# Kernel tuning notes

Measured on AMD Instinct MI355X. Metric: run time of the kernel, lower is better.

## Reference

```python
import jax, jax.numpy as jnp
import numpy as np

# Dimensions derived from LaneATTHead defaults (see shape_source)
B, CIN, CF, FH, FW = 8, 256, 64, 22, 40
A, S = 2784, 72          # n_anchors, n_offsets
NC = 2                   # num_category
D = CF * FH              # per-anchor feature dim = 1408
P = NC + 2 + 2 * S       # proposal dim = 148


def setup_inputs() -> dict:
    key = jax.random.key(0)
    ks = jax.random.split(key, 12)
    sc = 0.02
    return {
        "x": jax.random.normal(ks[0], (B, CIN, FH, FW), jnp.float32),
        "conv_w": jax.random.normal(ks[1], (CF, CIN), jnp.float32) * sc,
        "conv_b": jax.random.normal(ks[2], (CF,), jnp.float32) * sc,
        "attn_w": jax.random.normal(ks[3], (D, A - 1), jnp.float32) * sc,
        "attn_b": jax.random.normal(ks[4], (A - 1,), jnp.float32) * sc,
        "cls_w": jax.random.normal(ks[5], (2 * D, NC), jnp.float32) * sc,
        "cls_b": jax.random.normal(ks[6], (NC,), jnp.float32) * sc,
        "reg_w": jax.random.normal(ks[7], (2 * D, 2 * S), jnp.float32) * sc,
        "reg_b": jax.random.normal(ks[8], (2 * S,), jnp.float32) * sc,
        "anchors": jax.random.uniform(ks[9], (A, P), jnp.float32),
        "cut_xs": jax.random.randint(ks[10], (A, FH), 0, FW, jnp.int32),
        "invalid_mask": jax.random.randint(ks[11], (A, FH), 0, 2, jnp.int32).astype(jnp.bool_),
    }


def reference(x, conv_w, conv_b, attn_w, attn_b, cls_w, cls_b, reg_w, reg_b,
              anchors, cut_xs, invalid_mask):
    # 1x1 conv: [B,CIN,FH,FW] -> [B,CF,FH,FW]
    feats = jnp.einsum('bchw,oc->bohw', x, conv_w) + conv_b[None, :, None, None]

    # cut_anchor_features: gather per-anchor column per row, zero invalid
    rows = jnp.arange(FH)
    g = feats[:, :, rows[None, :], cut_xs]             # [B, CF, A, FH]
    g = jnp.transpose(g, (0, 2, 1, 3))                  # [B, A, CF, FH]
    g = jnp.where(invalid_mask[None, :, None, :], jnp.float32(0), g)
    baf = g.reshape(B, A, D)                            # [B, A, D]

    # attention over other anchors (softmax over A-1 slots)
    scores = baf @ attn_w + attn_b                      # [B, A, A-1]
    attention = jax.nn.softmax(scores, axis=-1)

    # scatter into [A,A] with zero diagonal (row-major off-diag fill, as in eye()+nonzero())
    i = jnp.arange(A)[:, None]
    k = jnp.arange(A - 1)[None, :]
    cols = k + (k >= i).astype(jnp.int32)               # [A, A-1]
    attn_mat = jnp.zeros((B, A, A), baf.dtype).at[:, i, cols].set(attention)

    # weighted pooling (equiv. of the transposed bmm chain)
    att_feat = jnp.einsum('bij,bjd->bid', attn_mat, baf)  # [B, A, D]

    f2 = jnp.concatenate([att_feat, baf], axis=-1)      # [B, A, 2D]
    cls = f2 @ cls_w + cls_b                            # [B, A, NC]
    reg = f2 @ reg_w + reg_b                            # [B, A, 2S]
    reg = jnp.concatenate([reg[..., :S], jax.nn.sigmoid(reg[..., S:])], axis=-1)

    base = jnp.broadcast_to(anchors, (B, A, P))
    # reg_proposals: [:, :, :NC]=cls ; [:, :, NC:NC+2]=anchor ; [:, :, NC+2:]+=reg
    props = jnp.concatenate([cls, base[..., NC:NC + 2], base[..., NC + 2:] + reg], axis=-1)
    return props, attn_mat
```

## Files before the change

kernel.cpp:

```cpp
#include <hip/hip_runtime.h>
#include <stdint.h>

typedef __attribute__((ext_vector_type(8))) __bf16 bf16x8;
typedef __attribute__((ext_vector_type(4))) float f32x4;
typedef __attribute__((ext_vector_type(2))) long long2v;
typedef unsigned short u16;
typedef unsigned char u8;

#define DEV static __device__ __forceinline__

constexpr int NB = 8;
constexpr int AA = 2784;
constexpr int AM1 = 2783;
constexpr int DD = 1408;
constexpr int MT = NB * AA;
constexpr int KP = 2816;

DEV u16 f2bf(float f) {
  uint32_t u = __builtin_bit_cast(uint32_t, f);
  u += 0x7FFFu + ((u >> 16) & 1u);
  return (u16)(u >> 16);
}
DEV float bf2f(unsigned v) { return __builtin_bit_cast(float, v << 16); }
DEV u8 f2f8(float f) {
  return (u8)(__builtin_amdgcn_cvt_pk_fp8_f32(f, f, 0, false) & 0xff);
}
DEV float4 cv4(unsigned w) {
  float4 r;
  r.x = __builtin_amdgcn_cvt_f32_fp8((int)w, 0);
  r.y = __builtin_amdgcn_cvt_f32_fp8((int)w, 1);
  r.z = __builtin_amdgcn_cvt_f32_fp8((int)w, 2);
  r.w = __builtin_amdgcn_cvt_f32_fp8((int)w, 3);
  return r;
}
DEV unsigned pk4(float a, float b, float c, float d) {
  int r = __builtin_amdgcn_cvt_pk_fp8_f32(a, b, 0, false);
  r = __builtin_amdgcn_cvt_pk_fp8_f32(c, d, r, true);
  return (unsigned)r;
}

DEV void load16_lds(const void* g, void* l) {
  auto gp = (const __attribute__((address_space(1))) uint32_t*)(uintptr_t)g;
  auto lp = (__attribute__((address_space(3))) uint32_t*)(uint32_t)(uintptr_t)l;
  __builtin_amdgcn_global_load_lds(gp, lp, 16, 0, 0);
}

#define VMW(n) asm volatile("s_waitcnt vmcnt(" #n ")" ::: "memory")
#define VMW0 asm volatile("s_waitcnt vmcnt(0)" ::: "memory")
#define LGK(n) asm volatile("s_waitcnt lgkmcnt(" #n ")" ::: "memory")
#define BARR asm volatile("s_barrier" ::: "memory")
#define SCHB __builtin_amdgcn_sched_barrier(0)

DEV void mf16c(f32x4 (&acc)[4][2], const long (&a)[4][2], const long (&b)[2][2]) {
  __builtin_amdgcn_s_setprio(1);
#pragma unroll
  for (int mt = 0; mt < 4; ++mt)
#pragma unroll
    for (int nt = 0; nt < 2; ++nt)
#pragma unroll
      for (int ks = 0; ks < 2; ++ks)
        acc[mt][nt] = __builtin_amdgcn_mfma_f32_16x16x32_fp8_fp8(
            a[mt][ks], b[nt][ks], acc[mt][nt], 0, 0, 0);
  __builtin_amdgcn_s_setprio(0);
}

template <int MODE>
__global__ __launch_bounds__(512, 4) void gemm_k(const u8* __restrict__ A,
                                                 const u8* __restrict__ Bt,
                                                 u8* __restrict__ out8,
                                                 u16* __restrict__ outh,
                                                 const float* __restrict__ bias1) {
  constexpr int K   = (MODE == 1) ? 1408 : KP;
  constexpr int NT  = K / 128;
  constexpr int LDA = (MODE == 1) ? 1408 : KP;
  constexpr int LDB = (MODE == 1) ? 1408 : KP;
  constexpr int MR  = (MODE == 1) ? MT : AA;
  constexpr int NRB = (MODE == 1) ? KP : 1408;
  __shared__ __align__(16) u8 As8[2][16384];
  __shared__ __align__(16) u8 Bs8[2][16384];
  const int tid = threadIdx.x;
  const int lane = tid & 63;
  const int w = tid >> 6;
  const int wr = w >> 2, wc = w & 3;
  const int l16 = lane & 15, lq = lane >> 4;
  const int l7 = l16 & 7;

  const int gx = gridDim.x, gy = gridDim.y;
  const int nwg = gx * gy;
  const int i = blockIdx.x + blockIdx.y * gx;
  const int xcd = i & 7, pos = i >> 3;
  const int q = nwg >> 3, r = nwg & 7;
  const int lid = (xcd < r ? xcd * (q + 1) : r * (q + 1) + (xcd - r) * q) + pos;
  const int m0 = (lid / gy) * 128, n0 = (lid % gy) * 128;

  const u8* Ab = A;
  const u8* Bb = Bt;
  u16* outp = outh;
  if constexpr (MODE == 2) {
    const int bz = blockIdx.z;
    Ab += (size_t)bz * AA * KP;
    Bb += (size_t)bz * DD * KP;
    outp += (size_t)bz * AA * DD;
  }

  auto stA = [&](int buf, int kt) {
#pragma unroll
    for (int inst = 0; inst < 2; ++inst) {
      int c = tid + inst * 512;
      int row = c >> 3, sl = c & 7;
      int sr = m0 + row;
      sr = sr < MR - 1 ? sr : MR - 1;
      load16_lds(Ab + (size_t)sr * LDA + kt * 128 + ((sl ^ (row & 7)) << 4),
                 &As8[buf][c << 4]);
    }
  };
  auto stB = [&](int buf, int kt) {
#pragma unroll
    for (int inst = 0; inst < 2; ++inst) {
      int c = tid + inst * 512;
      int row = c >> 3, sl = c & 7;
      int sr = n0 + row;
      sr = sr < NRB - 1 ? sr : NRB - 1;
      load16_lds(Bb + (size_t)sr * LDB + kt * 128 + ((sl ^ (row & 7)) << 4),
                 &Bs8[buf][c << 4]);
    }
  };
  auto rdA = [&](int buf, int kh, long (&a)[4][2]) {
    const int u = (kh * 4 + lq) ^ l7;
#pragma unroll
    for (int mt = 0; mt < 4; ++mt) {
      int rloc = wr * 64 + mt * 16 + l16;
      long2v v = *(const long2v*)&As8[buf][rloc * 128 + u * 16];
      a[mt][0] = v[0]; a[mt][1] = v[1];
    }
  };
  auto rdB = [&](int buf, int kh, long (&b)[2][2]) {
    const int u = (kh * 4 + lq) ^ l7;
#pragma unroll
    for (int nt = 0; nt < 2; ++nt) {
      int R = wc * 32 + nt * 16 + l16;
      long2v v = *(const long2v*)&Bs8[buf][R * 128 + u * 16];
      b[nt][0] = v[0]; b[nt][1] = v[1];
    }
  };

  f32x4 acc[4][2];
#pragma unroll
  for (int i2 = 0; i2 < 4; ++i2)
#pragma unroll
    for (int j = 0; j < 2; ++j) acc[i2][j] = 0.f;

  long a[4][2], bA[2][2], bB[2][2];

  stA(0, 0); stB(0, 0);
  stA(1, 1); stB(1, 1);
  VMW(4);
  BARR;

  for (int t = 0; t < NT; ++t) {
    const int cur = t & 1, nxt = cur ^ 1;
    if (t + 1 < NT) { stA(nxt, t + 1); stB(nxt, t + 1); }
    rdB(cur, 0, bA); rdA(cur, 0, a); rdB(cur, 1, bB);
    LGK(2); SCHB;
    mf16c(acc, a, bA);
    rdA(cur, 1, a);
    LGK(0); SCHB;
    mf16c(acc, a, bB);
    if (t + 1 < NT) { VMW0; BARR; }
  }

  if constexpr (MODE == 1) {
#pragma unroll
    for (int mi = 0; mi < 4; ++mi)
#pragma unroll
      for (int r2 = 0; r2 < 4; ++r2) {
        int m = m0 + wr * 64 + mi * 16 + lq * 4 + r2;
        int ii = m % AA;
#pragma unroll
        for (int ni = 0; ni < 2; ++ni) {
          int n = n0 + wc * 32 + ni * 16 + l16;
          if (n >= AM1) continue;
          int col = n + (n >= ii);
          out8[(size_t)m * KP + col] = f2f8(acc[mi][ni][r2] + bias1[n]);
        }
      }
  } else {
#pragma unroll
    for (int mi = 0; mi < 4; ++mi)
#pragma unroll
      for (int r2 = 0; r2 < 4; ++r2) {
        int m = m0 + wr * 64 + mi * 16 + lq * 4 + r2;
        if (m >= AA) continue;
        size_t base = (size_t)m * DD;
#pragma unroll
        for (int ni = 0; ni < 2; ++ni) {
          int n = n0 + wc * 32 + ni * 16 + l16;
          outp[base + n] = f2bf(acc[mi][ni][r2] * 0.00390625f);
        }
      }
  }
}

__global__ __launch_bounds__(256) void conv_k(const float* __restrict__ x,
                                              const float* __restrict__ w,
                                              const float* __restrict__ bias,
                                              float* __restrict__ feats) {
  __shared__ float xs[256 * 40];
  int bb = blockIdx.x / 22, h = blockIdx.x % 22;
  const float* xp = x + (size_t)bb * 256 * 880 + h * 40;
  for (int l = threadIdx.x; l < 256 * 40; l += 256)
    xs[l] = xp[(l / 40) * 880 + (l % 40)];
  __syncthreads();
  for (int l = threadIdx.x; l < 64 * 40; l += 256) {
    int o = l / 40, ww = l % 40;
    float acc = bias[o];
    const float* wr = w + o * 256;
#pragma unroll 8
    for (int c = 0; c < 256; ++c) acc += xs[c * 40 + ww] * wr[c];
    feats[((size_t)(bb * 64 + o) * 22 + h) * 40 + ww] = acc;
  }
}

__global__ __launch_bounds__(256) void gt_k(const float* __restrict__ feats,
                                            const int* __restrict__ cut,
                                            const u8* __restrict__ inv,
                                            u16* __restrict__ baf,
                                            u8* __restrict__ baf8,
                                            u8* __restrict__ bft8) {
  unsigned probe = 0;
#pragma unroll
  for (int t = 0; t < 10; ++t)
    probe |= (unsigned)inv[4 * t + 1] | (unsigned)inv[4 * t + 2] | (unsigned)inv[4 * t + 3];
  const bool is_u8 = (probe != 0);
  __shared__ u8 t8[64][65];
  int a0 = blockIdx.x * 64, d0 = blockIdx.y * 64, b = blockIdx.z;
  int tx = threadIdx.x & 63, ty = threadIdx.x >> 6;
  int d = d0 + tx, o = d / 22, h = d - o * 22;
  for (int r = ty; r < 64; r += 4) {
    int a = a0 + r;
    u8 f8 = 0;
    if (a < AA) {
      int msk = is_u8 ? (int)inv[a * 22 + h] : ((const int*)inv)[a * 22 + h];
      float v = 0.f;
      if (!msk) v = feats[((size_t)(b * 64 + o) * 22 + h) * 40 + cut[a * 22 + h]];
      baf[((size_t)b * AA + a) * DD + d] = f2bf(v);
      f8 = f2f8(v);
      baf8[((size_t)b * AA + a) * DD + d] = f8;
    }
    t8[r][tx] = f8;
  }
  __syncthreads();
  for (int r = ty; r < 64; r += 4) {
    int a = a0 + tx;
    if (a < AA) bft8[((size_t)b * DD + d0 + r) * KP + a] = t8[tx][r];
  }
}

__global__ __launch_bounds__(256) void tr_attw_k(const float* __restrict__ w,
                                                 u8* __restrict__ wt8) {
  __shared__ u8 t8[64][65];
  int n0 = blockIdx.x * 64, k0 = blockIdx.y * 64;
  int tx = threadIdx.x & 63, ty = threadIdx.x >> 6;
  for (int r = ty; r < 64; r += 4) {
    int n = n0 + tx;
    t8[r][tx] = (n < AM1) ? f2f8(w[(size_t)(k0 + r) * AM1 + n]) : (u8)0;
  }
  __syncthreads();
  for (int r = ty; r < 64; r += 4)
    wt8[(size_t)(n0 + r) * 1408 + k0 + tx] = t8[tx][r];
}

__global__ __launch_bounds__(256) void wt_k(const float* __restrict__ cw,
                                            const float* __restrict__ rw,
                                            u16* __restrict__ wt) {
  int n = blockIdx.x;
  for (int k = threadIdx.x; k < 2816; k += 256) {
    float v = 0.f;
    if (n < 2) v = cw[(size_t)k * 2 + n];
    else if (n < 146) v = rw[(size_t)k * 144 + (n - 2)];
    wt[(size_t)n * 2816 + k] = f2bf(v);
  }
}

__global__ __launch_bounds__(256) void softf_k(u8* __restrict__ attP) {
  const int row = blockIdx.x;
  const int i = row % AA;
  u8* p = attP + (size_t)row * KP;
  const int t = threadIdx.x;
  const bool act = (t < 176);
  uint4 qw = act ? ((const uint4*)p)[t] : make_uint4(0, 0, 0, 0);
  float v[16];
  { float4 f = cv4(qw.x); v[0] = f.x; v[1] = f.y; v[2] = f.z; v[3] = f.w; }
  { float4 f = cv4(qw.y); v[4] = f.x; v[5] = f.y; v[6] = f.z; v[7] = f.w; }
  { float4 f = cv4(qw.z); v[8] = f.x; v[9] = f.y; v[10] = f.z; v[11] = f.w; }
  { float4 f = cv4(qw.w); v[12] = f.x; v[13] = f.y; v[14] = f.z; v[15] = f.w; }
  const int base = t * 16;
  float mx = -3e38f;
#pragma unroll
  for (int e = 0; e < 16; ++e) {
    int j = base + e;
    if (act && j < AA && j != i) mx = fmaxf(mx, v[e]);
  }
#pragma unroll
  for (int o = 1; o < 64; o <<= 1) mx = fmaxf(mx, __shfl_xor(mx, o));
  __shared__ float rm[4], rs[4];
  if (!(t & 63)) rm[t >> 6] = mx;
  __syncthreads();
  mx = fmaxf(fmaxf(rm[0], rm[1]), fmaxf(rm[2], rm[3]));
  float s = 0.f, ev[16];
#pragma unroll
  for (int e = 0; e < 16; ++e) {
    int j = base + e;
    float tv = (act && j < AA && j != i) ? __expf(v[e] - mx) : 0.f;
    ev[e] = tv; s += tv;
  }
#pragma unroll
  for (int o = 1; o < 64; o <<= 1) s += __shfl_xor(s, o);
  if (!(t & 63)) rs[t >> 6] = s;
  __syncthreads();
  s = (rs[0] + rs[1]) + (rs[2] + rs[3]);
  const float inv = 256.f / s;
#pragma unroll
  for (int e = 0; e < 16; ++e) ev[e] *= inv;
  if (act) {
    uint4 ow;
    ow.x = pk4(ev[0], ev[1], ev[2], ev[3]);
    ow.y = pk4(ev[4], ev[5], ev[6], ev[7]);
    ow.z = pk4(ev[8], ev[9], ev[10], ev[11]);
    ow.w = pk4(ev[12], ev[13], ev[14], ev[15]);
    ((uint4*)p)[t] = ow;
  }
}

__global__ __launch_bounds__(256) void exp_k(const u8* __restrict__ src,
                                             float* __restrict__ dst) {
  int row = blockIdx.x;
  int t = threadIdx.x;
  if (t >= 174) return;
  uint4 qw = ((const uint4*)(src + (size_t)row * KP))[t];
  const float is = 0.00390625f;
  float4 f0 = cv4(qw.x), f1 = cv4(qw.y), f2 = cv4(qw.z), f3 = cv4(qw.w);
  float4* dp = (float4*)(dst + (size_t)row * AA + t * 16);
  dp[0] = make_float4(f0.x * is, f0.y * is, f0.z * is, f0.w * is);
  dp[1] = make_float4(f1.x * is, f1.y * is, f1.z * is, f1.w * is);
  dp[2] = make_float4(f2.x * is, f2.y * is, f2.z * is, f2.w * is);
  dp[3] = make_float4(f3.x * is, f3.y * is, f3.z * is, f3.w * is);
}

__global__ __launch_bounds__(256) void head_k(const u16* __restrict__ A1,
                                              const u16* __restrict__ A2,
                                              const u16* __restrict__ Bt,
                                              float* __restrict__ outf,
                                              const float* __restrict__ b1,
                                              const float* __restrict__ b2,
                                              const float* __restrict__ anch) {
  constexpr int K = 2816, NT = K / 32, BN = 160, HN = 80, NF = 5;
  __shared__ __align__(16) u16 As[2][128 * 32];
  __shared__ __align__(16) u16 Bs[2][BN * 32 + 512];
  const int tid = threadIdx.x;
  const int lane = tid & 63;
  const int wm = tid >> 7, wn = (tid >> 6) & 1;
  const int m0 = blockIdx.x * 128;
  const int l16 = lane & 15, lq = lane >> 4;

  auto stage = [&](int buf, int t) {
    const int k0 = t * 32;
    const u16* Asrc = (k0 < 1408) ? A1 : A2;
    const int kk = (k0 < 1408) ? k0 : k0 - 1408;
#pragma unroll
    for (int inst = 0; inst < 2; ++inst) {
      int c = tid + inst * 256;
      load16_lds(Asrc + (size_t)(m0 + (c >> 2)) * 1408 + kk + (c & 3) * 8, &As[buf][c * 8]);
    }
#pragma unroll
    for (int inst = 0; inst < 3; ++inst) {
      int c = tid + inst * 256;
      int ce = c < BN * 4 ? c : BN * 4 - 1;
      load16_lds(Bt + (size_t)(ce >> 2) * K + k0 + (ce & 3) * 8, &Bs[buf][ce * 8]);
    }
  };

  f32x4 acc[4][NF];
#pragma unroll
  for (int i = 0; i < 4; ++i)
#pragma unroll
    for (int j = 0; j < NF; ++j) acc[i][j] = 0.f;

  stage(0, 0);
  stage(1, 1);
  for (int t = 0; t < NT; ++t) {
    if (t + 1 < NT) VMW(5); else VMW0;
    BARR;
    const int cur = t & 1;
    bf16x8 av[4], bv[NF];
#pragma unroll
    for (int mt = 0; mt < 4; ++mt)
      av[mt] = *(const bf16x8*)&As[cur][(wm * 64 + mt * 16 + l16) * 32 + lq * 8];
#pragma unroll
    for (int nt = 0; nt < NF; ++nt)
      bv[nt] = *(const bf16x8*)&Bs[cur][(wn * HN + nt * 16 + l16) * 32 + lq * 8];
#pragma unroll
    for (int mt = 0; mt < 4; ++mt)
#pragma unroll
      for (int nt = 0; nt < NF; ++nt)
        acc[mt][nt] = __builtin_amdgcn_mfma_f32_16x16x32_bf16(av[mt], bv[nt], acc[mt][nt], 0, 0, 0);
    BARR;
    if (t + 2 < NT) stage(cur, t + 2);
  }

#pragma unroll
  for (int nt = 0; nt < NF; ++nt) {
    int n = wn * HN + nt * 16 + l16;
    if (n >= 146) continue;
#pragma unroll
    for (int mt = 0; mt < 4; ++mt)
#pragma unroll
      for (int r = 0; r < 4; ++r) {
        int m = m0 + wm * 64 + mt * 16 + lq * 4 + r;
        int ii = m % AA;
        float v = acc[mt][nt][r];
        if (n < 2) {
          outf[(size_t)m * 148 + n] = v + b1[n];
          if (n == 0) {
            outf[(size_t)m * 148 + 2] = anch[ii * 148 + 2];
            outf[(size_t)m * 148 + 3] = anch[ii * 148 + 3];
          }
        } else {
          int rr = n - 2;
          v += b2[rr];
          if (rr >= 72) v = 1.f / (1.f + __expf(-v));
          outf[(size_t)m * 148 + 4 + rr] = anch[ii * 148 + 4 + rr] + v;
        }
      }
  }
}

extern "C" void kernel_launch(void* const* d_in, const int* in_sizes, int n_in,
                              void* d_out, int out_size, void* d_ws, size_t ws_size,
                              hipStream_t stream) {
  const float* x       = (const float*)d_in[0];
  const float* conv_w  = (const float*)d_in[1];
  const float* conv_b  = (const float*)d_in[2];
  const float* attn_w  = (const float*)d_in[3];
  const float* attn_b  = (const float*)d_in[4];
  const float* cls_w   = (const float*)d_in[5];
  const float* cls_b   = (const float*)d_in[6];
  const float* reg_w   = (const float*)d_in[7];
  const float* reg_b   = (const float*)d_in[8];
  const float* anchors = (const float*)d_in[9];
  const int*   cut_xs  = (const int*)d_in[10];
  const u8*    inv     = (const u8*)d_in[11];

  float* props = (float*)d_out;
  float* attn  = props + (size_t)MT * 148;
  u16* attf = (u16*)attn;

  char* wp = (char*)d_ws;
  auto take = [&](size_t bytes) { char* p = wp; wp += (bytes + 255) & ~(size_t)255; return p; };
  u16* baf    = (u16*)take((size_t)MT * DD * 2);
  u8*  baf8   = (u8*)take((size_t)MT * DD);
  u8*  baft8  = (u8*)take((size_t)NB * DD * KP);
  u8*  attP8  = (u8*)take((size_t)MT * KP);
  u8*  attwt8 = (u8*)take((size_t)KP * 1408);
  float* feats = (float*)take((size_t)450560 * 4);
  u16* wt      = (u16*)take((size_t)160 * 2816 * 2);

  conv_k<<<dim3(176), 256, 0, stream>>>(x, conv_w, conv_b, feats);
  gt_k<<<dim3(44, 22, 8), 256, 0, stream>>>(feats, cut_xs, inv, baf, baf8, baft8);
  tr_attw_k<<<dim3(44, 22), 256, 0, stream>>>(attn_w, attwt8);
  wt_k<<<dim3(160), 256, 0, stream>>>(cls_w, reg_w, wt);

  gemm_k<1><<<dim3(174, 22), 512, 0, stream>>>(baf8, attwt8, attP8, nullptr, attn_b);
  softf_k<<<dim3(MT), 256, 0, stream>>>(attP8);
  gemm_k<2><<<dim3(22, 11, 8), 512, 0, stream>>>(attP8, baft8, nullptr, attf, nullptr);
  head_k<<<dim3(174), 256, 0, stream>>>(attf, baf, wt, props,
                                        cls_b, reg_b, anchors);
  exp_k<<<dim3(MT), 256, 0, stream>>>(attP8, attn);
}
```

Before: 601.8 us.

## Use 256-thread GEMM with 64x64 warp tiles; write half of attention output in softmax

The GEMM kernel moves from 512 threads with 64x32 per-warp tiles to 256 threads with 64x64 per-warp tiles. The block tile stays 128x128, so each wave holds more accumulators and reuses each LDS fragment more. Softmax now writes fp32 attention rows straight to the output for the first half of the rows. The bf16 scratch for the second GEMM moves into the second half of the attention output, and exp_k only expands that half afterward. This drops half of the fp8 re-read and expansion pass, but the larger register footprint lowers occupancy.

```diff
diff --git a/kernel.cpp b/kernel.cpp
--- a/kernel.cpp
+++ b/kernel.cpp
@@ -14,6 +14,7 @@
 constexpr int AM1 = 2783;
 constexpr int DD = 1408;
 constexpr int MT = NB * AA;
+constexpr int MH = MT / 2;
 constexpr int KP = 2816;
 
 DEV u16 f2bf(float f) {
@@ -51,12 +52,12 @@
 #define BARR asm volatile("s_barrier" ::: "memory")
 #define SCHB __builtin_amdgcn_sched_barrier(0)
 
-DEV void mf16c(f32x4 (&acc)[4][2], const long (&a)[4][2], const long (&b)[2][2]) {
+DEV void mf32c(f32x4 (&acc)[4][4], const long (&a)[4][2], const long (&b)[4][2]) {
   __builtin_amdgcn_s_setprio(1);
 #pragma unroll
   for (int mt = 0; mt < 4; ++mt)
 #pragma unroll
-    for (int nt = 0; nt < 2; ++nt)
+    for (int nt = 0; nt < 4; ++nt)
 #pragma unroll
       for (int ks = 0; ks < 2; ++ks)
         acc[mt][nt] = __builtin_amdgcn_mfma_f32_16x16x32_fp8_fp8(
@@ -65,7 +66,7 @@
 }
 
 template <int MODE>
-__global__ __launch_bounds__(512, 4) void gemm_k(const u8* __restrict__ A,
+__global__ __launch_bounds__(256, 2) void gemm_k(const u8* __restrict__ A,
                                                  const u8* __restrict__ Bt,
                                                  u8* __restrict__ out8,
                                                  u16* __restrict__ outh,
@@ -81,7 +82,7 @@
   const int tid = threadIdx.x;
   const int lane = tid & 63;
   const int w = tid >> 6;
-  const int wr = w >> 2, wc = w & 3;
+  const int wr = w >> 1, wc = w & 1;
   const int l16 = lane & 15, lq = lane >> 4;
   const int l7 = l16 & 7;
 
@@ -105,8 +106,8 @@
 
   auto stA = [&](int buf, int kt) {
 #pragma unroll
-    for (int inst = 0; inst < 2; ++inst) {
-      int c = tid + inst * 512;
+    for (int inst = 0; inst < 4; ++inst) {
+      int c = tid + inst * 256;
       int row = c >> 3, sl = c & 7;
       int sr = m0 + row;
       sr = sr < MR - 1 ? sr : MR - 1;
@@ -116,8 +117,8 @@
   };
   auto stB = [&](int buf, int kt) {
 #pragma unroll
-    for (int inst = 0; inst < 2; ++inst) {
-      int c = tid + inst * 512;
+    for (int inst = 0; inst < 4; ++inst) {
+      int c = tid + inst * 256;
       int row = c >> 3, sl = c & 7;
       int sr = n0 + row;
       sr = sr < NRB - 1 ? sr : NRB - 1;
@@ -134,38 +135,38 @@
       a[mt][0] = v[0]; a[mt][1] = v[1];
     }
   };
-  auto rdB = [&](int buf, int kh, long (&b)[2][2]) {
+  auto rdB = [&](int buf, int kh, long (&b)[4][2]) {
     const int u = (kh * 4 + lq) ^ l7;
 #pragma unroll
-    for (int nt = 0; nt < 2; ++nt) {
-      int R = wc * 32 + nt * 16 + l16;
+    for (int nt = 0; nt < 4; ++nt) {
+      int R = wc * 64 + nt * 16 + l16;
       long2v v = *(const long2v*)&Bs8[buf][R * 128 + u * 16];
       b[nt][0] = v[0]; b[nt][1] = v[1];
     }
   };
 
-  f32x4 acc[4][2];
+  f32x4 acc[4][4];
 #pragma unroll
   for (int i2 = 0; i2 < 4; ++i2)
 #pragma unroll
-    for (int j = 0; j < 2; ++j) acc[i2][j] = 0.f;
-
-  long a[4][2], bA[2][2], bB[2][2];
+    for (int j = 0; j < 4; ++j) acc[i2][j] = 0.f;
+
+  long a[4][2], bA[4][2], bB[4][2];
 
   stA(0, 0); stB(0, 0);
   stA(1, 1); stB(1, 1);
-  VMW(4);
+  VMW(8);
   BARR;
 
   for (int t = 0; t < NT; ++t) {
     const int cur = t & 1, nxt = cur ^ 1;
     if (t + 1 < NT) { stA(nxt, t + 1); stB(nxt, t + 1); }
     rdB(cur, 0, bA); rdA(cur, 0, a); rdB(cur, 1, bB);
-    LGK(2); SCHB;
-    mf16c(acc, a, bA);
+    LGK(4); SCHB;
+    mf32c(acc, a, bA);
     rdA(cur, 1, a);
     LGK(0); SCHB;
-    mf16c(acc, a, bB);
+    mf32c(acc, a, bB);
     if (t + 1 < NT) { VMW0; BARR; }
   }
 
@@ -177,8 +178,8 @@
         int m = m0 + wr * 64 + mi * 16 + lq * 4 + r2;
         int ii = m % AA;
 #pragma unroll
-        for (int ni = 0; ni < 2; ++ni) {
-          int n = n0 + wc * 32 + ni * 16 + l16;
+        for (int ni = 0; ni < 4; ++ni) {
+          int n = n0 + wc * 64 + ni * 16 + l16;
           if (n >= AM1) continue;
           int col = n + (n >= ii);
           out8[(size_t)m * KP + col] = f2f8(acc[mi][ni][r2] + bias1[n]);
@@ -193,8 +194,8 @@
         if (m >= AA) continue;
         size_t base = (size_t)m * DD;
 #pragma unroll
-        for (int ni = 0; ni < 2; ++ni) {
-          int n = n0 + wc * 32 + ni * 16 + l16;
+        for (int ni = 0; ni < 4; ++ni) {
+          int n = n0 + wc * 64 + ni * 16 + l16;
           outp[base + n] = f2bf(acc[mi][ni][r2] * 0.00390625f);
         }
       }
@@ -282,7 +283,8 @@
   }
 }
 
-__global__ __launch_bounds__(256) void softf_k(u8* __restrict__ attP) {
+__global__ __launch_bounds__(256) void softf_k(u8* __restrict__ attP,
+                                               float* __restrict__ fdst) {
   const int row = blockIdx.x;
   const int i = row % AA;
   u8* p = attP + (size_t)row * KP;
@@ -319,16 +321,24 @@
   if (!(t & 63)) rs[t >> 6] = s;
   __syncthreads();
   s = (rs[0] + rs[1]) + (rs[2] + rs[3]);
-  const float inv = 256.f / s;
+  const float inv = 1.f / s;
 #pragma unroll
   for (int e = 0; e < 16; ++e) ev[e] *= inv;
   if (act) {
+    const float sc = 256.f;
     uint4 ow;
-    ow.x = pk4(ev[0], ev[1], ev[2], ev[3]);
-    ow.y = pk4(ev[4], ev[5], ev[6], ev[7]);
-    ow.z = pk4(ev[8], ev[9], ev[10], ev[11]);
-    ow.w = pk4(ev[12], ev[13], ev[14], ev[15]);
+    ow.x = pk4(ev[0] * sc, ev[1] * sc, ev[2] * sc, ev[3] * sc);
+    ow.y = pk4(ev[4] * sc, ev[5] * sc, ev[6] * sc, ev[7] * sc);
+    ow.z = pk4(ev[8] * sc, ev[9] * sc, ev[10] * sc, ev[11] * sc);
+    ow.w = pk4(ev[12] * sc, ev[13] * sc, ev[14] * sc, ev[15] * sc);
     ((uint4*)p)[t] = ow;
+    if (row < MH && t < 174) {
+      float4* dp = (float4*)(fdst + (size_t)row * AA + base);
+      dp[0] = make_float4(ev[0], ev[1], ev[2], ev[3]);
+      dp[1] = make_float4(ev[4], ev[5], ev[6], ev[7]);
+      dp[2] = make_float4(ev[8], ev[9], ev[10], ev[11]);
+      dp[3] = make_float4(ev[12], ev[13], ev[14], ev[15]);
+    }
   }
 }
 
@@ -453,7 +463,7 @@
 
   float* props = (float*)d_out;
   float* attn  = props + (size_t)MT * 148;
-  u16* attf = (u16*)attn;
+  u16* attf = (u16*)(attn + (size_t)MH * AA);
 
   char* wp = (char*)d_ws;
   auto take = [&](size_t bytes) { char* p = wp; wp += (bytes + 255) & ~(size_t)255; return p; };
@@ -470,10 +480,10 @@
   tr_attw_k<<<dim3(44, 22), 256, 0, stream>>>(attn_w, attwt8);
   wt_k<<<dim3(160), 256, 0, stream>>>(cls_w, reg_w, wt);
 
-  gemm_k<1><<<dim3(174, 22), 512, 0, stream>>>(baf8, attwt8, attP8, nullptr, attn_b);
-  softf_k<<<dim3(MT), 256, 0, stream>>>(attP8);
-  gemm_k<2><<<dim3(22, 11, 8), 512, 0, stream>>>(attP8, baft8, nullptr, attf, nullptr);
+  gemm_k<1><<<dim3(174, 22), 256, 0, stream>>>(baf8, attwt8, attP8, nullptr, attn_b);
+  softf_k<<<dim3(MT), 256, 0, stream>>>(attP8, attn);
+  gemm_k<2><<<dim3(22, 11, 8), 256, 0, stream>>>(attP8, baft8, nullptr, attf, nullptr);
   head_k<<<dim3(174), 256, 0, stream>>>(attf, baf, wt, props,
                                         cls_b, reg_b, anchors);
-  exp_k<<<dim3(MT), 256, 0, stream>>>(attP8, attn);
-}
+  exp_k<<<dim3(MH), 256, 0, stream>>>(attP8 + (size_t)MH * KP, attn + (size_t)MH * AA);
+}
```

Result: slower. 649.5 us (+7.9%).
